# Kernel tuning notes

Hardware: AMD Instinct MI355X
Metric: run time of the kernel (lower is better)

Reference implementation:

```python
import jax, jax.numpy as jnp
import numpy as np

N = 20000   # nodes
E = 320000  # edges (before self loops)
IN = 128    # in_channel
H = 8       # heads
C = 128     # out_channels per head
HC = H * C  # 1024
G = 64      # graphs in batch


def _w(k, shape):
    s = 1.0 / np.sqrt(shape[-1])
    return jax.random.uniform(k, shape, jnp.float32, -s, s)


def setup_inputs() -> dict:
    key = jax.random.key(0)
    ks = jax.random.split(key, 12)
    return {
        "x": jax.random.normal(ks[0], (N, IN), jnp.float32),
        "edge_index": jax.random.randint(ks[1], (2, E), 0, N, dtype=jnp.int64),
        "batch": jnp.sort(jax.random.randint(ks[2], (N,), 0, G, dtype=jnp.int64)),
        # GATv2Conv params
        "Wl": _w(ks[3], (HC, IN)), "bl": jnp.zeros((HC,), jnp.float32),
        "Wr": _w(ks[4], (HC, IN)), "br": jnp.zeros((HC,), jnp.float32),
        "att": _w(ks[5], (H, C)),
        "Wres": _w(ks[6], (HC, IN)),
        "bias_conv": jnp.zeros((HC,), jnp.float32),
        # post-attention Linear(HC -> C)
        "Wlin": _w(ks[7], (C, HC)), "blin": jnp.zeros((C,), jnp.float32),
        # MLP head 128 -> 16 -> 32 -> 5
        "W1": _w(ks[8], (16, C)), "b1": jnp.zeros((16,), jnp.float32),
        "W2": _w(ks[9], (32, 16)), "b2": jnp.zeros((32,), jnp.float32),
        "W3": _w(ks[10], (5, 32)), "b3": jnp.zeros((5,), jnp.float32),
    }


def reference(x, edge_index, batch, Wl, bl, Wr, br, att, Wres, bias_conv,
              Wlin, blin, W1, b1, W2, b2, W3, b3):
    # --- GATv2Conv (PyG semantics: add_self_loops=True, concat=True, residual) ---
    loops = jnp.arange(N)
    src = jnp.concatenate([edge_index[0], loops])  # [E+N]
    dst = jnp.concatenate([edge_index[1], loops])
    x_l = (x @ Wl.T + bl).reshape(N, H, C)
    x_r = (x @ Wr.T + br).reshape(N, H, C)
    # per-edge attention logits
    e = jax.nn.leaky_relu(x_l[src] + x_r[dst], 0.2)        # [E+N, H, C]
    logits = jnp.einsum('ehc,hc->eh', e, att)              # [E+N, H]
    # segment softmax over destination neighborhoods
    m = jax.ops.segment_max(logits, dst, num_segments=N)
    a = jnp.exp(logits - m[dst])
    denom = jax.ops.segment_sum(a, dst, num_segments=N)
    alpha = a / (denom[dst] + 1e-16)                       # [E+N, H]
    # scatter-add weighted messages
    out = jax.ops.segment_sum(x_l[src] * alpha[:, :, None], dst,
                              num_segments=N).reshape(N, HC)
    out = out + x @ Wres.T + bias_conv                     # residual + bias
    # --- Linear + ELU ---
    h = jax.nn.elu(out @ Wlin.T + blin)                    # [N, C]
    # --- global mean pool per graph ---
    cnt = jax.ops.segment_sum(jnp.ones((N,), h.dtype), batch, num_segments=G)
    pooled = jax.ops.segment_sum(h, batch, num_segments=G) / jnp.maximum(cnt, 1.0)[:, None]
    # --- MLP head ---
    y = jax.nn.relu(pooled @ W1.T + b1)
    y = jax.nn.relu(y @ W2.T + b2)
    return y @ W3.T + b3                                   # [G, 5]
```

## Files before the change

### kernel.cpp

```cpp
#include <hip/hip_runtime.h>
#include <hip/hip_bf16.h>
#include <math.h>

#define N_NODES 20000
#define N_EDGES 320000
#define IN_CH   128
#define HEADS   8
#define CPH     128
#define HCH     1024
#define NG      64
#define ETOT    (N_EDGES + N_NODES)
#define NCVT    768
#define NROWT   157
#define GRID_P  (NROWT * 16)
#define PL      ((size_t)N_NODES * 128)

typedef __attribute__((ext_vector_type(8))) short s8v;
typedef __attribute__((ext_vector_type(4))) float f4v;
typedef __attribute__((ext_vector_type(8))) float f8v;
typedef __attribute__((ext_vector_type(4))) unsigned short u16x4;
typedef __attribute__((ext_vector_type(8))) unsigned short u16x8;

__device__ __forceinline__ unsigned short bf16_rne(float f) {
    unsigned u = __float_as_uint(f);
    unsigned r = u + 0x7fffu + ((u >> 16) & 1u);
    return (unsigned short)(r >> 16);
}
__device__ __forceinline__ float bf16_to_f(unsigned short h) {
    return __uint_as_float((unsigned)h << 16);
}

__global__ void init_kernel(int* __restrict__ deg, float* __restrict__ pooled) {
    int i = blockIdx.x * blockDim.x + threadIdx.x;
    if (i < N_NODES) deg[i] = 0;
    if (i < NG * CPH) pooled[i] = 0.0f;
}

__global__ void cvt_all(const float* __restrict__ x,  const float* __restrict__ Wl,
                        const float* __restrict__ Wr, const float* __restrict__ Wlin,
                        unsigned short* __restrict__ xhi,  unsigned short* __restrict__ xlo,
                        unsigned short* __restrict__ wlhi, unsigned short* __restrict__ wllo,
                        unsigned short* __restrict__ wrhi, unsigned short* __restrict__ wrlo,
                        unsigned short* __restrict__ wnhi, unsigned short* __restrict__ wnlo,
                        const int* __restrict__ ei, int* __restrict__ deg,
                        const float* __restrict__ Wres, const float* __restrict__ bias_conv,
                        const float* __restrict__ blin,
                        unsigned short* __restrict__ wchi, unsigned short* __restrict__ wclo,
                        float* __restrict__ bcomb)
{
    const int t = threadIdx.x;
    if (blockIdx.x < NCVT) {
        const int NX = N_NODES * IN_CH, NW = HCH * IN_CH;
        const int TOT4 = (NX + 3 * NW) >> 2;
        const int stride = NCVT * 256;
        for (int q = blockIdx.x * 256 + t; q < TOT4; q += stride) {
            int i = q << 2;
            const float* s; unsigned short *hi, *lo; int k;
            if (i < NX)               { s = x;    hi = xhi;  lo = xlo;  k = i; }
            else if (i < NX + NW)     { s = Wl;   hi = wlhi; lo = wllo; k = i - NX; }
            else if (i < NX + 2 * NW) { s = Wr;   hi = wrhi; lo = wrlo; k = i - NX - NW; }
            else                      { s = Wlin; hi = wnhi; lo = wnlo; k = i - NX - 2 * NW; }
            f4v f = *(const f4v*)&s[k];
            u16x4 h, l;
            #pragma unroll
            for (int e = 0; e < 4; ++e) {
                unsigned short hh = bf16_rne(f[e]);
                h[e] = hh;
                l[e] = bf16_rne(f[e] - bf16_to_f(hh));
            }
            *(u16x4*)&hi[k] = h;
            *(u16x4*)&lo[k] = l;
        }
        for (int e = blockIdx.x * 256 + t; e < ETOT; e += stride) {
            int dst = (e < N_EDGES) ? ei[N_EDGES + e] : (e - N_EDGES);
            atomicAdd(&deg[dst], 1);
        }
    } else if (t < 128) {
        const int j = blockIdx.x - NCVT;
        float s = 0.0f, pb = 0.0f;
        for (int m = 0; m < HCH; ++m) {
            float wl = Wlin[j * HCH + m];
            s  += wl * Wres[m * IN_CH + t];
            pb += wl * bias_conv[m];
        }
        unsigned short h = bf16_rne(s);
        wchi[j * IN_CH + t] = h;
        wclo[j * IN_CH + t] = bf16_rne(s - bf16_to_f(h));
        if (t == 0) bcomb[j] = blin[j] + pb;
    }
}

__global__ __launch_bounds__(256) void proj_gemm(
    const unsigned short* __restrict__ Ahi,
    const unsigned short* __restrict__ WLhi, const unsigned short* __restrict__ WLlo,
    const unsigned short* __restrict__ WRhi, const unsigned short* __restrict__ WRlo,
    const float* __restrict__ bl, const float* __restrict__ br,
    const float* __restrict__ att,
    unsigned short* __restrict__ xl_h, unsigned short* __restrict__ xr_h,
    float* __restrict__ dl, float* __restrict__ dr, int M)
{
    __shared__ unsigned short cst[128][136];
    const int id  = blockIdx.x;
    const int nat = (id & 7) * (GRID_P / 8) + (id >> 3);
    const int bx  = nat >> 4;
    const int by  = nat & 15;
    const int t    = threadIdx.x;
    const int wave = t >> 6, lane = t & 63;
    const int wr = wave >> 1, wc = wave & 1;
    const int l15 = lane & 15, lg = lane >> 4;
    const int m0 = bx * 128 + wr * 64;
    const int sel = by >> 3;
    const int hh  = by & 7;
    const int col0 = hh * 128;
    const unsigned short* Whi = sel ? WRhi : WLhi;
    const unsigned short* Wlo = sel ? WRlo : WLlo;
    const float* bias = sel ? br : bl;
    unsigned short* C = sel ? xr_h : xl_h;
    float* D = sel ? dr : dl;
    const int koff = lg * 8;
    const int K = IN_CH;

    int rowA[4], colB[4];
    #pragma unroll
    for (int i = 0; i < 4; ++i) { int r = m0 + i * 16 + l15; rowA[i] = r < M ? r : M - 1; }
    #pragma unroll
    for (int j = 0; j < 4; ++j) colB[j] = col0 + wc * 64 + j * 16 + l15;

    float bj[4];
    #pragma unroll
    for (int j = 0; j < 4; ++j) bj[j] = bias[colB[j]];

    f4v acc[4][4];
    #pragma unroll
    for (int i = 0; i < 4; ++i)
        #pragma unroll
        for (int j = 0; j < 4; ++j) acc[i][j] = (f4v){0.f, 0.f, 0.f, 0.f};

    for (int k0 = 0; k0 < K; k0 += 32) {
        s8v ah[4], bh[4], blv[4];
        #pragma unroll
        for (int i = 0; i < 4; ++i)
            ah[i] = *(const s8v*)&Ahi[(size_t)rowA[i] * K + k0 + koff];
        #pragma unroll
        for (int j = 0; j < 4; ++j) {
            size_t off = (size_t)colB[j] * K + k0 + koff;
            bh[j]  = *(const s8v*)&Whi[off];
            blv[j] = *(const s8v*)&Wlo[off];
        }
        #pragma unroll
        for (int i = 0; i < 4; ++i)
            #pragma unroll
            for (int j = 0; j < 4; ++j) {
                acc[i][j] = __builtin_amdgcn_mfma_f32_16x16x32_bf16(ah[i], bh[j],  acc[i][j], 0, 0, 0);
                acc[i][j] = __builtin_amdgcn_mfma_f32_16x16x32_bf16(ah[i], blv[j], acc[i][j], 0, 0, 0);
            }
    }

    #pragma unroll
    for (int i = 0; i < 4; ++i)
        #pragma unroll
        for (int r = 0; r < 4; ++r) {
            int lr = wr * 64 + i * 16 + lg * 4 + r;
            #pragma unroll
            for (int j = 0; j < 4; ++j)
                cst[lr][wc * 64 + j * 16 + l15] = bf16_rne(acc[i][j][r] + bj[j]);
        }
    __syncthreads();

    {
        const int c8  = (t & 15) * 8;
        const int r16 = t >> 4;
        #pragma unroll
        for (int it = 0; it < 8; ++it) {
            int lr = it * 16 + r16;
            int row = bx * 128 + lr;
            if (row >= M) continue;
            u16x8 v = *(const u16x8*)&cst[lr][c8];
            *(u16x8*)&C[(size_t)hh * PL + (size_t)row * 128 + c8] = v;
        }
    }

    {
        const int r2  = t >> 1;
        const int ch0 = (t & 1) * 64;
        float q = 0.0f;
        #pragma unroll
        for (int c = 0; c < 64; c += 8) {
            u16x8 cv = *(const u16x8*)&cst[r2][ch0 + c];
            f4v a0 = *(const f4v*)&att[hh * 128 + ch0 + c];
            f4v a1 = *(const f4v*)&att[hh * 128 + ch0 + c + 4];
            q = fmaf(a0[0], bf16_to_f(cv[0]), q);
            q = fmaf(a0[1], bf16_to_f(cv[1]), q);
            q = fmaf(a0[2], bf16_to_f(cv[2]), q);
            q = fmaf(a0[3], bf16_to_f(cv[3]), q);
            q = fmaf(a1[0], bf16_to_f(cv[4]), q);
            q = fmaf(a1[1], bf16_to_f(cv[5]), q);
            q = fmaf(a1[2], bf16_to_f(cv[6]), q);
            q = fmaf(a1[3], bf16_to_f(cv[7]), q);
        }
        q += __shfl_xor(q, 1, 64);
        int row = bx * 128 + r2;
        if ((t & 1) == 0 && row < M) D[hh * N_NODES + row] = q;
    }
}

__global__ __launch_bounds__(128) void mfma_gemm2(
    const unsigned short* __restrict__ A1h,
    const unsigned short* __restrict__ B1hi, const unsigned short* __restrict__ B1lo, int K1,
    const unsigned short* __restrict__ A2hi, const unsigned short* __restrict__ A2lo,
    const unsigned short* __restrict__ B2hi, const unsigned short* __restrict__ B2lo, int K2,
    const float* __restrict__ bias, const int* __restrict__ batch,
    float* __restrict__ pooled, int M)
{
    __shared__ float cst[32][130];
    __shared__ int batch_s[32];
    const int t    = threadIdx.x;
    const int wc   = t >> 6, lane = t & 63;
    const int l15 = lane & 15, lg = lane >> 4;
    const int m0 = blockIdx.x * 32;
    const int n0 = wc * 64;
    const int koff = lg * 8;

    if (t < 32) {
        int row = m0 + t;
        batch_s[t] = (row < M) ? batch[row] : -1;
    }

    int rowA[2], colB[4];
    #pragma unroll
    for (int i = 0; i < 2; ++i) { int r = m0 + i * 16 + l15; rowA[i] = r < M ? r : M - 1; }
    #pragma unroll
    for (int j = 0; j < 4; ++j) colB[j] = n0 + j * 16 + l15;

    float bj[4];
    #pragma unroll
    for (int j = 0; j < 4; ++j) bj[j] = bias[colB[j]];

    f4v acc[2][4];
    #pragma unroll
    for (int i = 0; i < 2; ++i)
        #pragma unroll
        for (int j = 0; j < 4; ++j) acc[i][j] = (f4v){0.f, 0.f, 0.f, 0.f};

    for (int k0 = 0; k0 < K1; k0 += 32) {
        s8v ah[2], bh[4], blv[4];
        #pragma unroll
        for (int i = 0; i < 2; ++i)
            ah[i] = *(const s8v*)&A1h[(size_t)rowA[i] * K1 + k0 + koff];
        #pragma unroll
        for (int j = 0; j < 4; ++j) {
            size_t off = (size_t)colB[j] * K1 + k0 + koff;
            bh[j]  = *(const s8v*)&B1hi[off];
            blv[j] = *(const s8v*)&B1lo[off];
        }
        #pragma unroll
        for (int i = 0; i < 2; ++i)
            #pragma unroll
            for (int j = 0; j < 4; ++j) {
                acc[i][j] = __builtin_amdgcn_mfma_f32_16x16x32_bf16(ah[i], bh[j],  acc[i][j], 0, 0, 0);
                acc[i][j] = __builtin_amdgcn_mfma_f32_16x16x32_bf16(ah[i], blv[j], acc[i][j], 0, 0, 0);
            }
    }
    for (int k0 = 0; k0 < K2; k0 += 32) {
        s8v ah[2], al[2], bh[4], blv[4];
        #pragma unroll
        for (int i = 0; i < 2; ++i) {
            size_t off = (size_t)rowA[i] * K2 + k0 + koff;
            ah[i] = *(const s8v*)&A2hi[off];
            al[i] = *(const s8v*)&A2lo[off];
        }
        #pragma unroll
        for (int j = 0; j < 4; ++j) {
            size_t off = (size_t)colB[j] * K2 + k0 + koff;
            bh[j]  = *(const s8v*)&B2hi[off];
            blv[j] = *(const s8v*)&B2lo[off];
        }
        #pragma unroll
        for (int i = 0; i < 2; ++i)
            #pragma unroll
            for (int j = 0; j < 4; ++j) {
                acc[i][j] = __builtin_amdgcn_mfma_f32_16x16x32_bf16(ah[i], bh[j],  acc[i][j], 0, 0, 0);
                acc[i][j] = __builtin_amdgcn_mfma_f32_16x16x32_bf16(ah[i], blv[j], acc[i][j], 0, 0, 0);
                acc[i][j] = __builtin_amdgcn_mfma_f32_16x16x32_bf16(al[i], bh[j],  acc[i][j], 0, 0, 0);
            }
    }

    #pragma unroll
    for (int i = 0; i < 2; ++i)
        #pragma unroll
        for (int r = 0; r < 4; ++r) {
            int lr = i * 16 + lg * 4 + r;
            #pragma unroll
            for (int j = 0; j < 4; ++j) {
                float v = acc[i][j][r] + bj[j];
                v = v > 0.0f ? v : expm1f(v);
                cst[lr][n0 + j * 16 + l15] = v;
            }
        }
    __syncthreads();

    const int col = t;
    if (col < 128) {
        float run = 0.0f;
        int cur_g = -2;
        #pragma unroll 4
        for (int r = 0; r < 32; ++r) {
            int g = batch_s[r];
            if (g != cur_g) {
                if (cur_g >= 0) atomicAdd(&pooled[cur_g * CPH + col], run);
                run = 0.0f; cur_g = g;
            }
            if (g >= 0) run += cst[r][col];
        }
        if (cur_g >= 0) atomicAdd(&pooled[cur_g * CPH + col], run);
    }
}

__global__ __launch_bounds__(256) void scan_kernel(
    const int* __restrict__ deg, int* __restrict__ rowptr, int* __restrict__ wof)
{
    __shared__ int wsum[4];
    __shared__ int carry_s;
    const int t = threadIdx.x, wave = t >> 6, lane = t & 63;
    if (t == 0) { carry_s = 0; rowptr[0] = 0; }
    __syncthreads();
    for (int base = 0; base < N_NODES; base += 1024) {
        int idx = base + t * 4;
        int d[4], p[4];
        #pragma unroll
        for (int k = 0; k < 4; ++k)
            d[k] = (idx + k < N_NODES) ? deg[idx + k] : 0;
        p[0] = d[0]; p[1] = p[0] + d[1]; p[2] = p[1] + d[2]; p[3] = p[2] + d[3];
        int v = p[3];
        #pragma unroll
        for (int off = 1; off < 64; off <<= 1) {
            int u = __shfl_up(v, off, 64);
            if (lane >= off) v += u;
        }
        if (lane == 63) wsum[wave] = v;
        __syncthreads();
        int woff = carry_s;
        #pragma unroll
        for (int w = 0; w < 4; ++w) if (w < wave) woff += wsum[w];
        int tbase = woff + v - p[3];
        #pragma unroll
        for (int k = 0; k < 4; ++k) {
            if (idx + k < N_NODES) {
                rowptr[idx + k + 1] = tbase + p[k];
                wof[idx + k] = tbase + p[k] - d[k];
            }
        }
        __syncthreads();
        if (t == 255) carry_s = woff + v;
        __syncthreads();
    }
}

__global__ void scatter_kernel(const int* __restrict__ ei, int* __restrict__ wof,
                               int* __restrict__ csr_src)
{
    for (int e = blockIdx.x * blockDim.x + threadIdx.x; e < ETOT;
         e += gridDim.x * blockDim.x) {
        int src, dst;
        if (e < N_EDGES) { src = ei[e]; dst = ei[N_EDGES + e]; }
        else             { src = dst = e - N_EDGES; }
        int p = atomicAdd(&wof[dst], 1);
        csr_src[p] = src;
    }
}

__global__ __launch_bounds__(256) void agg_fused(
    const unsigned short* __restrict__ xl_h, const unsigned short* __restrict__ xr_h,
    const float* __restrict__ att,
    const float* __restrict__ dl, const float* __restrict__ dr,
    const int* __restrict__ rowptr, const int* __restrict__ csr_src,
    unsigned short* __restrict__ agg_h)
{
    __shared__ float lds_m[128], lds_s[128];
    __shared__ float lds_acc[8][128];
    const int dst = blockIdx.x;
    const int t = threadIdx.x;
    const int grp = t >> 7;
    const int u = t & 127;
    const int h = u >> 4;
    const int c16 = (u & 15) * 8;
    const size_t pbase = (size_t)h * PL + c16;
    const int beg = rowptr[dst], end = rowptr[dst + 1];

    const u16x8 bh8 = *(const u16x8*)&xr_h[pbase + (size_t)dst * 128];
    f8v b;
    #pragma unroll
    for (int e = 0; e < 8; ++e) b[e] = bf16_to_f(bh8[e]);
    f8v w04;
    {
        f4v a0 = *(const f4v*)&att[u * 8];
        f4v a1 = *(const f4v*)&att[u * 8 + 4];
        #pragma unroll
        for (int e = 0; e < 4; ++e) { w04[e] = 0.4f * a0[e]; w04[e + 4] = 0.4f * a1[e]; }
    }
    const float pb = 0.6f * dr[h * N_NODES + dst];

    float m = -__builtin_inff(), s = 0.0f;
    f8v acc = {0.f, 0.f, 0.f, 0.f, 0.f, 0.f, 0.f, 0.f};

    int j = beg + grp * 2;
    for (; j + 1 < end; j += 4) {
        const int s0 = csr_src[j], s1 = csr_src[j + 1];
        const u16x8 vh0 = *(const u16x8*)&xl_h[pbase + (size_t)s0 * 128];
        const u16x8 vh1 = *(const u16x8*)&xl_h[pbase + (size_t)s1 * 128];
        const float d0 = dl[h * N_NODES + s0], d1 = dl[h * N_NODES + s1];
        f8v v0, v1;
        #pragma unroll
        for (int e = 0; e < 8; ++e) { v0[e] = bf16_to_f(vh0[e]); v1[e] = bf16_to_f(vh1[e]); }

        float q0 = w04[0] * __builtin_fabsf(v0[0] + b[0]);
        float q1 = w04[0] * __builtin_fabsf(v1[0] + b[0]);
        #pragma unroll
        for (int e = 1; e < 8; ++e) {
            q0 = fmaf(w04[e], __builtin_fabsf(v0[e] + b[e]), q0);
            q1 = fmaf(w04[e], __builtin_fabsf(v1[e] + b[e]), q1);
        }
        #pragma unroll
        for (int off = 8; off; off >>= 1) {
            q0 += __shfl_xor(q0, off, 16);
            q1 += __shfl_xor(q1, off, 16);
        }
        const float p0 = fmaf(0.6f, d0, q0) + pb;
        const float p1 = fmaf(0.6f, d1, q1) + pb;

        const float mx = fmaxf(p0, p1);
        if (mx > m) {
            float scale = __expf(m - mx);
            float e0 = __expf(p0 - mx), e1 = __expf(p1 - mx);
            s = s * scale + e0 + e1;
            acc = acc * scale + v0 * e0 + v1 * e1;
            m = mx;
        } else {
            float e0 = __expf(p0 - m), e1 = __expf(p1 - m);
            s += e0 + e1;
            acc += v0 * e0 + v1 * e1;
        }
    }
    if (j < end) {
        const int s0 = csr_src[j];
        const u16x8 vh0 = *(const u16x8*)&xl_h[pbase + (size_t)s0 * 128];
        const float d0 = dl[h * N_NODES + s0];
        f8v v0;
        #pragma unroll
        for (int e = 0; e < 8; ++e) v0[e] = bf16_to_f(vh0[e]);
        float q0 = w04[0] * __builtin_fabsf(v0[0] + b[0]);
        #pragma unroll
        for (int e = 1; e < 8; ++e)
            q0 = fmaf(w04[e], __builtin_fabsf(v0[e] + b[e]), q0);
        #pragma unroll
        for (int off = 8; off; off >>= 1) q0 += __shfl_xor(q0, off, 16);
        const float p0 = fmaf(0.6f, d0, q0) + pb;
        if (p0 > m) {
            float scale = __expf(m - p0);
            s = s * scale + 1.0f;
            acc = acc * scale + v0;
            m = p0;
        } else {
            float e0 = __expf(p0 - m);
            s += e0;
            acc += v0 * e0;
        }
    }

    if (grp == 1) {
        lds_m[u] = m;
        lds_s[u] = s;
        #pragma unroll
        for (int e = 0; e < 8; ++e) lds_acc[e][u] = acc[e];
    }
    __syncthreads();
    if (grp == 0) {
        const float m1 = lds_m[u], s1 = lds_s[u];
        const float M  = fmaxf(m, m1);
        const float c0 = __expf(m - M);
        const float c1 = __expf(m1 - M);
        const float S  = s * c0 + s1 * c1;
        const float inv = 1.0f / (S + 1e-16f);
        u16x8 hv;
        #pragma unroll
        for (int e = 0; e < 8; ++e) {
            float r = (acc[e] * c0 + lds_acc[e][u] * c1) * inv;
            hv[e] = bf16_rne(r);
        }
        *(u16x8*)&agg_h[(size_t)dst * HCH + u * 8] = hv;
    }
}

__global__ __launch_bounds__(128) void head_kernel(
    const float* __restrict__ pooled, const int* __restrict__ batch,
    const float* __restrict__ W1, const float* __restrict__ b1,
    const float* __restrict__ W2, const float* __restrict__ b2,
    const float* __restrict__ W3, const float* __restrict__ b3,
    float* __restrict__ out)
{
    __shared__ float sm_pool[128];
    __shared__ float sm_y1[16];
    __shared__ float sm_y2[32];
    const int g = blockIdx.x;
    const int t = threadIdx.x;

    int lo = 0, hi = N_NODES;
    while (lo < hi) { int mid = (lo + hi) >> 1; if (batch[mid] <  g) lo = mid + 1; else hi = mid; }
    const int s0 = lo;
    hi = N_NODES;
    while (lo < hi) { int mid = (lo + hi) >> 1; if (batch[mid] <= g) lo = mid + 1; else hi = mid; }
    const float inv = 1.0f / fmaxf((float)(lo - s0), 1.0f);

    sm_pool[t] = pooled[g * CPH + t] * inv;
    __syncthreads();

    {
        const int j  = t >> 3;
        const int c0 = (t & 7) * 16;
        float s = 0.0f;
        #pragma unroll
        for (int k = 0; k < 16; k += 4) {
            f4v wv = *(const f4v*)&W1[j * CPH + c0 + k];
            f4v pv = *(const f4v*)&sm_pool[c0 + k];
            s = fmaf(wv[0], pv[0], s); s = fmaf(wv[1], pv[1], s);
            s = fmaf(wv[2], pv[2], s); s = fmaf(wv[3], pv[3], s);
        }
        s += __shfl_xor(s, 1, 8);
        s += __shfl_xor(s, 2, 8);
        s += __shfl_xor(s, 4, 8);
        if ((t & 7) == 0) sm_y1[j] = fmaxf(s + b1[j], 0.0f);
    }
    __syncthreads();

    if (t < 32) {
        float s = b2[t];
        #pragma unroll
        for (int k = 0; k < 16; ++k) s = fmaf(W2[t * 16 + k], sm_y1[k], s);
        sm_y2[t] = fmaxf(s, 0.0f);
    }
    __syncthreads();

    if (t < 5) {
        float s = b3[t];
        #pragma unroll
        for (int k = 0; k < 32; ++k) s = fmaf(W3[t * 32 + k], sm_y2[k], s);
        out[g * 5 + t] = s;
    }
}

extern "C" void kernel_launch(void* const* d_in, const int* in_sizes, int n_in,
                              void* d_out, int out_size, void* d_ws, size_t ws_size,
                              hipStream_t stream)
{
    const float* x         = (const float*)d_in[0];
    const int*   ei        = (const int*)  d_in[1];
    const int*   batch     = (const int*)  d_in[2];
    const float* Wl        = (const float*)d_in[3];
    const float* bl        = (const float*)d_in[4];
    const float* Wr        = (const float*)d_in[5];
    const float* br        = (const float*)d_in[6];
    const float* att       = (const float*)d_in[7];
    const float* Wres      = (const float*)d_in[8];
    const float* bias_conv = (const float*)d_in[9];
    const float* Wlin      = (const float*)d_in[10];
    const float* blin      = (const float*)d_in[11];
    const float* W1        = (const float*)d_in[12];
    const float* b1        = (const float*)d_in[13];
    const float* W2        = (const float*)d_in[14];
    const float* b2        = (const float*)d_in[15];
    const float* W3        = (const float*)d_in[16];
    const float* b3        = (const float*)d_in[17];
    float* out = (float*)d_out;

    unsigned short* xl_h  = (unsigned short*)d_ws;
    unsigned short* xr_h  = xl_h + (size_t)N_NODES * HCH;
    unsigned short* agg_h = xr_h + (size_t)N_NODES * HCH;
    float* pooled = (float*)(agg_h + (size_t)N_NODES * HCH);
    float* bcomb  = pooled + NG * CPH;
    float* dl     = bcomb + 128;
    float* dr     = dl + (size_t)N_NODES * 8;
    unsigned short* x_hi  = (unsigned short*)(dr + (size_t)N_NODES * 8);
    unsigned short* x_lo  = x_hi  + (size_t)N_NODES * IN_CH;
    unsigned short* wl_hi = x_lo  + (size_t)N_NODES * IN_CH;
    unsigned short* wl_lo = wl_hi + HCH * IN_CH;
    unsigned short* wr_hi = wl_lo + HCH * IN_CH;
    unsigned short* wr_lo = wr_hi + HCH * IN_CH;
    unsigned short* wn_hi = wr_lo + HCH * IN_CH;
    unsigned short* wn_lo = wn_hi + CPH * HCH;
    unsigned short* wc_hi = wn_lo + CPH * HCH;
    unsigned short* wc_lo = wc_hi + CPH * IN_CH;
    int* deg     = (int*)(wc_lo + CPH * IN_CH);
    int* rowptr  = deg + N_NODES;
    int* wof     = rowptr + N_NODES + 1;
    int* csr_src = wof + N_NODES;

    init_kernel<<<(N_NODES + 255) / 256, 256, 0, stream>>>(deg, pooled);

    cvt_all<<<NCVT + 128, 256, 0, stream>>>(x, Wl, Wr, Wlin,
                                            x_hi, x_lo, wl_hi, wl_lo,
                                            wr_hi, wr_lo, wn_hi, wn_lo,
                                            ei, deg,
                                            Wres, bias_conv, blin,
                                            wc_hi, wc_lo, bcomb);

    proj_gemm<<<GRID_P, 256, 0, stream>>>(x_hi, wl_hi, wl_lo, wr_hi, wr_lo,
                                          bl, br, att, xl_h, xr_h, dl, dr, N_NODES);

    scan_kernel<<<1, 256, 0, stream>>>(deg, rowptr, wof);
    scatter_kernel<<<1024, 256, 0, stream>>>(ei, wof, csr_src);

    agg_fused<<<N_NODES, 256, 0, stream>>>(xl_h, xr_h, att, dl, dr,
                                           rowptr, csr_src, agg_h);

    dim3 g2((N_NODES + 31) / 32, 1);
    mfma_gemm2<<<g2, 128, 0, stream>>>(agg_h, wn_hi, wn_lo, HCH,
                                       x_hi, x_lo, wc_hi, wc_lo, IN_CH,
                                       bcomb, batch, pooled, N_NODES);

    head_kernel<<<NG, 128, 0, stream>>>(pooled, batch, W1, b1, W2, b2, W3, b3, out);
}
```

Measured before the change: 363.8 us.

## Remap aggregation blocks to head-major tiles of 16 destination nodes

The aggregation kernel previously ran one block per destination node, with two 128-thread groups splitting that node's edges and merging their online-softmax state through shared memory after a barrier. Now each block handles one head for 16 destination nodes, with 16 threads per node walking all of that node's edges alone. This removes the LDS merge and __syncthreads, and keeps each block's gathers within one head plane, which may improve cache locality. In exchange, per-node edge parallelism drops, so load imbalance from varying degrees can leave threads in a wavefront idle.

Result: faster. 348.6 us (-4.2%).

```diff
diff --git a/kernel.cpp b/kernel.cpp
--- a/kernel.cpp
+++ b/kernel.cpp
@@ -376,15 +376,14 @@
     const int* __restrict__ rowptr, const int* __restrict__ csr_src,
     unsigned short* __restrict__ agg_h)
 {
-    __shared__ float lds_m[128], lds_s[128];
-    __shared__ float lds_acc[8][128];
-    const int dst = blockIdx.x;
+    const int bid = blockIdx.x;
+    const int h     = bid & 7;
+    const int chunk = bid >> 3;
     const int t = threadIdx.x;
-    const int grp = t >> 7;
-    const int u = t & 127;
-    const int h = u >> 4;
-    const int c16 = (u & 15) * 8;
-    const size_t pbase = (size_t)h * PL + c16;
+    const int dg = t >> 4;
+    const int l  = t & 15;
+    const int dst = chunk * 16 + dg;
+    const size_t pbase = (size_t)h * PL + l * 8;
     const int beg = rowptr[dst], end = rowptr[dst + 1];
 
     const u16x8 bh8 = *(const u16x8*)&xr_h[pbase + (size_t)dst * 128];
@@ -393,8 +392,8 @@
     for (int e = 0; e < 8; ++e) b[e] = bf16_to_f(bh8[e]);
     f8v w04;
     {
-        f4v a0 = *(const f4v*)&att[u * 8];
-        f4v a1 = *(const f4v*)&att[u * 8 + 4];
+        f4v a0 = *(const f4v*)&att[h * 128 + l * 8];
+        f4v a1 = *(const f4v*)&att[h * 128 + l * 8 + 4];
         #pragma unroll
         for (int e = 0; e < 4; ++e) { w04[e] = 0.4f * a0[e]; w04[e + 4] = 0.4f * a1[e]; }
     }
@@ -403,8 +402,8 @@
     float m = -__builtin_inff(), s = 0.0f;
     f8v acc = {0.f, 0.f, 0.f, 0.f, 0.f, 0.f, 0.f, 0.f};
 
-    int j = beg + grp * 2;
-    for (; j + 1 < end; j += 4) {
+    int j = beg;
+    for (; j + 1 < end; j += 2) {
         const int s0 = csr_src[j], s1 = csr_src[j + 1];
         const u16x8 vh0 = *(const u16x8*)&xl_h[pbase + (size_t)s0 * 128];
         const u16x8 vh1 = *(const u16x8*)&xl_h[pbase + (size_t)s1 * 128];
@@ -467,28 +466,12 @@
         }
     }
 
-    if (grp == 1) {
-        lds_m[u] = m;
-        lds_s[u] = s;
-        #pragma unroll
-        for (int e = 0; e < 8; ++e) lds_acc[e][u] = acc[e];
-    }
-    __syncthreads();
-    if (grp == 0) {
-        const float m1 = lds_m[u], s1 = lds_s[u];
-        const float M  = fmaxf(m, m1);
-        const float c0 = __expf(m - M);
-        const float c1 = __expf(m1 - M);
-        const float S  = s * c0 + s1 * c1;
-        const float inv = 1.0f / (S + 1e-16f);
-        u16x8 hv;
-        #pragma unroll
-        for (int e = 0; e < 8; ++e) {
-            float r = (acc[e] * c0 + lds_acc[e][u] * c1) * inv;
-            hv[e] = bf16_rne(r);
-        }
-        *(u16x8*)&agg_h[(size_t)dst * HCH + u * 8] = hv;
-    }
+    const float inv = 1.0f / (s + 1e-16f);
+    f8v r = acc * inv;
+    u16x8 hv;
+    #pragma unroll
+    for (int e = 0; e < 8; ++e) hv[e] = bf16_rne(r[e]);
+    *(u16x8*)&agg_h[(size_t)dst * HCH + h * 128 + l * 8] = hv;
 }
 
 __global__ __launch_bounds__(128) void head_kernel(
@@ -609,8 +592,8 @@
     scan_kernel<<<1, 256, 0, stream>>>(deg, rowptr, wof);
     scatter_kernel<<<1024, 256, 0, stream>>>(ei, wof, csr_src);
 
-    agg_fused<<<N_NODES, 256, 0, stream>>>(xl_h, xr_h, att, dl, dr,
-                                           rowptr, csr_src, agg_h);
+    agg_fused<<<HEADS * (N_NODES / 16), 256, 0, stream>>>(xl_h, xr_h, att, dl, dr,
+                                                          rowptr, csr_src, agg_h);
 
     dim3 g2((N_NODES + 31) / 32, 1);
     mfma_gemm2<<<g2, 128, 0, stream>>>(agg_h, wn_hi, wn_lo, HCH,
```
